# Kernel optimization log

Hardware: AMD Instinct MI355X
Metric: run time of the kernel (lower is better)

## Reference

```python
import jax, jax.numpy as jnp
import numpy as np

NUM_CLASSES = 7
CLASS_WEIGHT = 1.0
BOX_WEIGHT = 1.0


def _linear_sum_assignment(cost):
    """Exact Hungarian via shortest augmenting paths (Jonker-Volgenant style).
    Matches scipy.optimize.linear_sum_assignment for rectangular matrices:
    returns (row_ind, col_ind) of length min(n, m), row_ind sorted ascending."""
    C = np.asarray(cost, dtype=np.float64)
    transposed = C.shape[0] > C.shape[1]
    if transposed:
        C = C.T
    n, m = C.shape  # n <= m
    u = np.zeros(n + 1)
    v = np.zeros(m + 1)
    p = np.zeros(m + 1, dtype=np.int64)    # p[j]: row matched to col j (1-based); 0 = free
    way = np.zeros(m + 1, dtype=np.int64)
    for i in range(1, n + 1):
        p[0] = i
        j0 = 0
        minv = np.full(m + 1, np.inf)
        used = np.zeros(m + 1, dtype=bool)
        while True:
            used[j0] = True
            i0 = p[j0]
            cur = C[i0 - 1] - u[i0] - v[1:]
            free = ~used[1:]
            better = free & (cur < minv[1:])
            minv[1:][better] = cur[better]
            way[1:][better] = j0
            masked = np.where(free, minv[1:], np.inf)
            j0n = int(np.argmin(masked)) + 1
            delta = masked[j0n - 1]
            uj = np.nonzero(used)[0]
            u[p[uj]] += delta
            v[uj] -= delta
            minv[1:][free] -= delta
            j0 = j0n
            if p[j0] == 0:
                break
        while j0 != 0:   # augment along alternating path
            j1 = way[j0]
            p[j0] = p[j1]
            j0 = j1
    cols = np.nonzero(p[1:] > 0)[0]
    rows = p[1:][cols] - 1
    if transposed:
        rows, cols = cols, rows
    order = np.argsort(rows)
    return rows[order], cols[order]


def _cost_matrices(pred_logits, pred_boxes, gt_labels, gt_boxes):
    """Batched cost: class_weight * (-log_softmax gathered at gt labels) + box_weight * L1 cdist on xyz."""
    B, Q, _ = pred_logits.shape
    M = gt_labels.shape[1]
    log_probs = jax.nn.log_softmax(pred_logits, axis=-1)                       # (B,Q,C)
    idx = jnp.broadcast_to(gt_labels[:, None, :], (B, Q, M))
    class_cost = -jnp.take_along_axis(log_probs, idx, axis=2)                  # (B,Q,M)
    box_cost = jnp.sum(jnp.abs(pred_boxes[:, :, None, :3] - gt_boxes[:, None, :, :3]), axis=-1)  # (B,Q,M)
    return CLASS_WEIGHT * class_cost + BOX_WEIGHT * box_cost


def _matched_loss(pred_logits, pred_boxes, gt_labels, gt_boxes, rows, cols):
    B = pred_logits.shape[0]
    bidx = jnp.arange(B)[:, None]
    ml = pred_logits[bidx, rows]          # (B,M,C) matched logits
    mb = pred_boxes[bidx, rows]           # (B,M,7) matched boxes
    gl = gt_labels[bidx, cols]            # (B,M)
    gb = gt_boxes[bidx, cols]             # (B,M,7)
    logp = jax.nn.log_softmax(ml, axis=-1)
    ce = -jnp.mean(jnp.take_along_axis(logp, gl[..., None], axis=-1)[..., 0], axis=1)  # (B,)
    l1 = jnp.mean(jnp.abs(mb - gb), axis=(1, 2))                                       # (B,)
    return jnp.mean(CLASS_WEIGHT * ce + BOX_WEIGHT * l1)


def setup_inputs() -> dict:
    key = jax.random.key(0)
    k1, k2, k3, k4 = jax.random.split(key, 4)
    B, Q, M = 128, 900, 100
    return {
        'pred_logits': jax.random.normal(k1, (B, Q, NUM_CLASSES), dtype=jnp.float32),
        'pred_boxes': jax.random.normal(k2, (B, Q, 7), dtype=jnp.float32),
        'gt_labels': jax.random.randint(k3, (B, M), 0, NUM_CLASSES, dtype=jnp.int32),
        'gt_boxes': jax.random.normal(k4, (B, M, 7), dtype=jnp.float32),
    }


def reference(pred_logits, pred_boxes, gt_labels, gt_boxes):
    B = pred_logits.shape[0]
    M = gt_labels.shape[1]
    # Assignment is done on detached costs (host-side), matching the original module.
    cost = np.asarray(_cost_matrices(pred_logits, pred_boxes, gt_labels, gt_boxes))
    rows = np.zeros((B, M), dtype=np.int64)
    cols = np.zeros((B, M), dtype=np.int64)
    for b in range(B):
        r, c = _linear_sum_assignment(cost[b])
        rows[b], cols[b] = r, c
    return _matched_loss(pred_logits, pred_boxes, gt_labels, gt_boxes,
                         jnp.asarray(rows), jnp.asarray(cols))
```

## Files before the change

kernel.cpp:

```cpp
#include <hip/hip_runtime.h>
#include <math.h>


#define NQ   900
#define NG   100
#define NC   7
#define CPL  15
#define ROUNDS 10
#define INFF __builtin_inff()

__device__ __forceinline__ float readlane_f(float x, int l) {
  return __int_as_float(__builtin_amdgcn_readlane(__float_as_int(x), l));
}

template<int CTRL>
__device__ __forceinline__ void dpp_amin_step(float &v, int &ix) {
  float v2 = __int_as_float(__builtin_amdgcn_update_dpp(
      __float_as_int(v), __float_as_int(v), CTRL, 0xf, 0xf, false));
  int i2 = __builtin_amdgcn_update_dpp(ix, ix, CTRL, 0xf, 0xf, false);
  ix = (v2 < v) ? i2 : ix;
  v  = fminf(v, v2);
}
__device__ __forceinline__ void wave_amin_b(float v, int ix, float &ov, int &oi) {
  dpp_amin_step<0x111>(v, ix);
  dpp_amin_step<0x112>(v, ix);
  dpp_amin_step<0x114>(v, ix);
  dpp_amin_step<0x118>(v, ix);
  dpp_amin_step<0x142>(v, ix);
  dpp_amin_step<0x143>(v, ix);
  ov = readlane_f(v, 63);
  oi = __builtin_amdgcn_readlane(ix, 63);
}

template<int CTRL>
__device__ __forceinline__ void dpp_amin2_step(float &a, int &ia, float &b, int &ib) {
  const int INFI = 0x7f800000;
  float a2 = __int_as_float(__builtin_amdgcn_update_dpp(
      INFI, __float_as_int(a), CTRL, 0xf, 0xf, false));
  float b2 = __int_as_float(__builtin_amdgcn_update_dpp(
      INFI, __float_as_int(b), CTRL, 0xf, 0xf, false));
  int ia2 = __builtin_amdgcn_update_dpp(0, ia, CTRL, 0xf, 0xf, false);
  int ib2 = __builtin_amdgcn_update_dpp(0, ib, CTRL, 0xf, 0xf, false);
  bool sw = a2 < a;
  float hi = sw ? a  : a2;  int ihi = sw ? ia  : ia2;
  float lo = sw ? a2 : a;   int ilo = sw ? ia2 : ia;
  bool t1 = b2 < b;
  float bb = t1 ? b2 : b;   int ibb = t1 ? ib2 : ib;
  bool t2 = hi < bb;
  b = t2 ? hi : bb;         ib = t2 ? ihi : ibb;
  a = lo; ia = ilo;
}
__device__ __forceinline__ void wave_amin2_b(float a, int ia, float b, int ib,
    float &o1, int &oc1, float &o2, int &oc2) {
  dpp_amin2_step<0x111>(a, ia, b, ib);
  dpp_amin2_step<0x112>(a, ia, b, ib);
  dpp_amin2_step<0x114>(a, ia, b, ib);
  dpp_amin2_step<0x118>(a, ia, b, ib);
  dpp_amin2_step<0x142>(a, ia, b, ib);
  dpp_amin2_step<0x143>(a, ia, b, ib);
  o1 = readlane_f(a, 63); oc1 = __builtin_amdgcn_readlane(ia, 63);
  o2 = readlane_f(b, 63); oc2 = __builtin_amdgcn_readlane(ib, 63);
}

template<int CTRL>
__device__ __forceinline__ float dpp_add_step(float x) {
  int y = __builtin_amdgcn_update_dpp(0, __float_as_int(x),
                                      CTRL, 0xf, 0xf, true);
  return x + __int_as_float(y);
}
__device__ __forceinline__ float wave_sum_b(float x) {
  x = dpp_add_step<0x111>(x);
  x = dpp_add_step<0x112>(x);
  x = dpp_add_step<0x114>(x);
  x = dpp_add_step<0x118>(x);
  x = dpp_add_step<0x142>(x);
  x = dpp_add_step<0x143>(x);
  return __int_as_float(__builtin_amdgcn_readlane(__float_as_int(x), 63));
}
__device__ __forceinline__ void gl_lds16(const float* g, float* lds_base) {
  __builtin_amdgcn_global_load_lds(
      (const __attribute__((address_space(1))) unsigned int*)g,
      (__attribute__((address_space(3))) unsigned int*)lds_base, 16, 0, 0);
}
__device__ __forceinline__ float sel7v(float a0,float a1,float a2,float a3,
                                       float a4,float a5,float a6,int lab){
  float r = a0;
  r = lab==1 ? a1 : r;  r = lab==2 ? a2 : r;  r = lab==3 ? a3 : r;
  r = lab==4 ? a4 : r;  r = lab==5 ? a5 : r;  r = lab==6 ? a6 : r;
  return r;
}

__global__ __launch_bounds__(256, 1) void hungarian_fused_kernel(
    const float* __restrict__ logits, const float* __restrict__ pboxes,
    const int* __restrict__ glabels, const float* __restrict__ gboxes,
    float* __restrict__ out, float inv_B)
{
  const int b = blockIdx.x, tid = threadIdx.x;
  const int lane = tid & 63, w = tid >> 6;

  __shared__ __align__(16) float s_raw[NQ * NC];
  __shared__ __align__(16) float s_nlpT[NC * 1024];
  __shared__ __align__(16) float s_pb[960 * NC];
  __shared__ __align__(16) float s_gb[NG * NC];
  __shared__ __align__(16) int   s_glab[NG];
  __shared__ float s_u[NG + 1];
  __shared__ float s_v[CPL * 64];
  __shared__ int   s_p[NQ];
  __shared__ unsigned s_bid[NQ];
  __shared__ int   s_rmatch[NG];
  __shared__ float s_bm1[NG], s_bm2[NG];
  __shared__ int   s_bc[NG];
  __shared__ unsigned long long s_fm[2];
  __shared__ float s_f1v[NG]; __shared__ int s_f1c[NG];
  __shared__ float s_f2v[NG]; __shared__ int s_f2c[NG];
  __shared__ int   s_mlist[128];

  {
    const float* Lg = logits + (size_t)b * NQ * NC;
    const float* Pg = pboxes + (size_t)b * NQ * NC;
    const float* Gg = gboxes + (size_t)b * NG * NC;
    const int*   Bg = glabels + (size_t)b * NG;
    #pragma unroll
    for (int t = 0; t < 7; t++) {
      int i = (t << 8) + tid;
      if (i < (NQ * NC) / 4) {
        gl_lds16(Lg + i * 4, s_raw + ((t << 8) + (w << 6)) * 4);
        gl_lds16(Pg + i * 4, s_pb  + ((t << 8) + (w << 6)) * 4);
      }
    }
    if (tid < (NG * NC) / 4) gl_lds16(Gg + tid * 4, s_gb + (w << 6) * 4);
    if (tid < NG / 4) gl_lds16((const float*)Bg + tid * 4, (float*)s_glab);
    for (int i = tid; i < (960 - NQ) * NC; i += 256) s_pb[NQ * NC + i] = 0.f;
    for (int c = tid; c < NQ; c += 256) { s_p[c] = 0x7fffffff; s_bid[c] = 0xFFFFFFFFu; }
    for (int i = tid; i < CPL * 64; i += 256) s_v[i] = 0.f;
    if (tid == 0) s_u[0] = 0.f;
  }
  __syncthreads();

  for (int i = tid; i < 960; i += 256) {
    int L = i & 63, t = i >> 6;
    int q = L * CPL + t;
    float o[NC];
    if (q < NQ) {
      float x[NC];
      #pragma unroll
      for (int c = 0; c < NC; c++) x[c] = s_raw[q * NC + c];
      float mx = x[0];
      #pragma unroll
      for (int c = 1; c < NC; c++) mx = fmaxf(mx, x[c]);
      float tt[NC]; float se = 0.f;
      #pragma unroll
      for (int c = 0; c < NC; c++) { tt[c] = x[c] - mx; se += __expf(tt[c]); }
      float lg = __logf(se);
      #pragma unroll
      for (int c = 0; c < NC; c++) o[c] = lg - tt[c];
    } else {
      #pragma unroll
      for (int c = 0; c < NC; c++) o[c] = INFF;
    }
    #pragma unroll
    for (int c = 0; c < NC; c++) s_nlpT[c * 1024 + t * 64 + L] = o[c];
  }
  __syncthreads();

  const bool lval = (lane < NQ / CPL);
  float cpx[CPL], cpy[CPL], cpz[CPL];
  #pragma unroll
  for (int t = 0; t < CPL; t++) {
    int c = lane * CPL + t;
    cpx[t]=s_pb[c*NC+0]; cpy[t]=s_pb[c*NC+1]; cpz[t]=s_pb[c*NC+2];
  }

  for (int rl = 0; rl < 25; rl++) {
    int r = w * 25 + rl;
    int lab = s_glab[r];
    float gx = s_gb[r*NC+0], gy = s_gb[r*NC+1], gz = s_gb[r*NC+2];
    float m1 = INFF; int c1t = 0;
    #pragma unroll
    for (int t = 0; t < CPL; t++) {
      float nl = s_nlpT[lab*1024 + t*64 + lane];
      float bs = fabsf(cpx[t]-gx)+fabsf(cpy[t]-gy)+fabsf(cpz[t]-gz);
      float cost = nl + bs;
      bool lt1 = cost < m1;
      c1t = lt1 ? t : c1t;
      m1 = fminf(m1, cost);
    }
    float w1; int col;
    wave_amin_b(m1, lane * CPL + c1t, w1, col);
    if (lane == 0) {
      s_u[r + 1] = w1;
      s_bc[r] = col;
      atomicMin(&s_p[col], r + 1);
    }
  }
  __syncthreads();
  for (int c = tid; c < NQ; c += 256) if (s_p[c] == 0x7fffffff) s_p[c] = 0;
  if (tid < NG) {
    int c = s_bc[tid];
    s_rmatch[tid] = (s_p[c] == tid + 1) ? c + 1 : 0;
  }
  __syncthreads();

  for (int round = 0; round < ROUNDS; round++) {
    if (w == 0) {
      unsigned long long m = __ballot(s_rmatch[lane] == 0);
      if (lane == 0) s_fm[0] = m;
    } else if (w == 1) {
      unsigned long long m = __ballot((lane < NG - 64) && s_rmatch[64 + lane] == 0);
      if (lane == 0) s_fm[1] = m;
    }
    __syncthreads();
    const unsigned long long fm0r = s_fm[0], fm1r = s_fm[1];
    if ((fm0r | fm1r) == 0) break;
    float vreg[CPL];
    #pragma unroll
    for (int t = 0; t < CPL; t++) vreg[t] = s_v[t*64 + lane];
    {
      unsigned long long mm0 = fm0r, mm1 = fm1r;
      int idx = 0;
      while (mm0 | mm1) {
        int r;
        if (mm0) { int b2 = (int)__builtin_ctzll(mm0); mm0 &= mm0 - 1; r = b2; }
        else     { int b2 = (int)__builtin_ctzll(mm1); mm1 &= mm1 - 1; r = 64 + b2; }
        if ((idx++ & 3) != w) continue;
        int lab = s_glab[r];
        float gx = s_gb[r*NC+0], gy = s_gb[r*NC+1], gz = s_gb[r*NC+2];
        float m1 = INFF, m2 = INFF; int c1t = 0;
        #pragma unroll
        for (int t = 0; t < CPL; t++) {
          float nl = s_nlpT[lab*1024 + t*64 + lane];
          float bs = fabsf(cpx[t]-gx)+fabsf(cpy[t]-gy)+fabsf(cpz[t]-gz);
          float cost = (nl + bs) - vreg[t];
          bool lt1 = cost < m1;
          m2 = lt1 ? m1 : fminf(m2, cost);
// ... 78 lines not shown
                                : ((ff1 >> (tid - 64)) & 1ull);
      if (wasfree) {
        int c = s_bc[tid];
        if (s_p[c] == 0) atomicMin(&s_bid[c], (unsigned)tid);
      }
    }
    __syncthreads();
    if (tid < NG) {
      bool wasfree = (tid < 64) ? ((ff0 >> tid) & 1ull)
                                : ((ff1 >> (tid - 64)) & 1ull);
      if (wasfree) {
        int c = s_bc[tid];
        if (s_p[c] == 0 && s_bid[c] == (unsigned)tid) {
          s_p[c] = tid + 1;
          s_rmatch[tid] = c + 1;
        }
      }
    }
    __syncthreads();
    if (w == 0) {
      unsigned long long m = __ballot(s_rmatch[lane] == 0);
      if (lane == 0) s_fm[0] = m;
    } else if (w == 1) {
      unsigned long long m = __ballot((lane < NG - 64) && s_rmatch[64 + lane] == 0);
      if (lane == 0) s_fm[1] = m;
    }
    __syncthreads();
  }

  const unsigned long long gg0 = s_fm[0], gg1 = s_fm[1];
  const int nf2 = __popcll(gg0) + __popcll(gg1);

  if (nf2 > 0) {
  unsigned fmask = 0;
  if (lval) {
    #pragma unroll
    for (int t = 0; t < CPL; t++)
      if (s_p[lane * CPL + t] == 0) fmask |= (1u << t);
  }

  auto top2row = [&](int lab, float gx, float gy, float gz,
                     float &o1v, int &o1c, float &o2v, int &o2c) {
    float m1 = INFF, m2 = INFF; int c1 = 0, c2 = 0;
    #pragma unroll
    for (int t = 0; t < CPL; t++) {
      float nl = s_nlpT[lab*1024 + t*64 + lane];
      float bs = fabsf(cpx[t]-gx)+fabsf(cpy[t]-gy)+fabsf(cpz[t]-gz);
      float cost = nl + bs;
      cost = ((fmask >> t) & 1u) ? cost : INFF;
      bool lt1 = cost < m1;
      bool lt2 = cost < m2;
      c2 = lt1 ? c1 : (lt2 ? t : c2);
      m2 = lt1 ? m1 : fminf(m2, cost);
      c1 = lt1 ? t : c1;
      m1 = fminf(m1, cost);
    }
    wave_amin2_b(m1, lane * CPL + c1, m2, lane * CPL + c2, o1v, o1c, o2v, o2c);
  };

  for (int rl = 0; rl < 25; rl++) {
    int r = w * 25 + rl;
    int lab = s_glab[r];
    float gx = s_gb[r*NC+0], gy = s_gb[r*NC+1], gz = s_gb[r*NC+2];
    float v1, v2; int cc1, cc2;
    top2row(lab, gx, gy, gz, v1, cc1, v2, cc2);
    if (lane == 0) {
      s_f1v[r] = v1; s_f1c[r] = cc1; s_f2v[r] = v2; s_f2c[r] = cc2;
    }
  }
  __syncthreads();
  if (w != 0) return;

  volatile float* vu = s_u;

  const bool r1ok = (lane < NG - 64);
  int   rlab0 = s_glab[lane];
  float rgx0 = s_gb[lane*NC+0], rgy0 = s_gb[lane*NC+1], rgz0 = s_gb[lane*NC+2];
  int   rlab1 = 0; float rgx1=0.f, rgy1=0.f, rgz1=0.f;
  if (r1ok) {
    int r = 64 + lane;
    rlab1 = s_glab[r];
    rgx1 = s_gb[r*NC+0]; rgy1 = s_gb[r*NC+1]; rgz1 = s_gb[r*NC+2];
  }
  float ru0 = vu[lane + 1];
  float ru1 = r1ok ? vu[lane + 65] : 0.f;
  float rf1v0 = s_f1v[lane];       int rf1c0 = s_f1c[lane];
  float rf2v0 = s_f2v[lane];       int rf2c0 = s_f2c[lane];
  float rf1v1 = r1ok ? s_f1v[64+lane] : INFF; int rf1c1 = r1ok ? s_f1c[64+lane] : -1;
  float rf2v1 = r1ok ? s_f2v[64+lane] : INFF; int rf2c1 = r1ok ? s_f2c[64+lane] : -1;

  unsigned long long fm0 = gg0;
  unsigned long long fm1 = gg1;

  int NM = 0;
  #pragma unroll
  for (int t = 0; t < CPL; t++) {
    int c = lane * CPL + t;
    bool has = lval && (s_p[c] > 0);
    unsigned long long m = __ballot(has);
    int pos = NM + (int)__popcll(m & ((1ull << lane) - 1ull));
    if (has) s_mlist[pos] = c;
    NM += (int)__popcll(m);
  }

// ... 142 lines not shown
      ru0 = vu[lane + 1];
      if (r1ok) ru1 = vu[lane + 65];
      #pragma unroll
      for (int k = 0; k < 2; k++)
        if ((lane + (k << 6)) < NM) mpu[k] = vu[mprow[k]];

      if (lane == (jf / CPL)) fmask &= ~(1u << (jf - (jf / CPL) * CPL));
      if (rf1c0 == jf) { rf1v0 = rf2v0; rf1c0 = rf2c0; rf2c0 = -1; rf2v0 = INFF; }
      else if (rf2c0 == jf) { rf2c0 = -1; rf2v0 = INFF; }
      if (rf1c1 == jf) { rf1v1 = rf2v1; rf1c1 = rf2c1; rf2c1 = -1; rf2v1 = INFF; }
      else if (rf2c1 == jf) { rf2c1 = -1; rf2v1 = INFF; }
      unsigned long long need0 = __ballot(rf1c0 < 0);
      unsigned long long need1 = __ballot(r1ok && (rf1c1 < 0));
      while (need0) {
        int rb = (int)__builtin_ctzll(need0); need0 &= need0 - 1;
        int lab = __builtin_amdgcn_readlane(rlab0, rb);
        float gx = readlane_f(rgx0, rb), gy = readlane_f(rgy0, rb), gz = readlane_f(rgz0, rb);
        float v1, v2; int cc1, cc2;
        top2row(lab, gx, gy, gz, v1, cc1, v2, cc2);
        if (lane == rb) { rf1v0=v1; rf1c0=cc1; rf2v0=v2; rf2c0=cc2; }
      }
      while (need1) {
        int rb = (int)__builtin_ctzll(need1); need1 &= need1 - 1;
        int lab = __builtin_amdgcn_readlane(rlab1, rb);
        float gx = readlane_f(rgx1, rb), gy = readlane_f(rgy1, rb), gz = readlane_f(rgz1, rb);
        float v1, v2; int cc1, cc2;
        top2row(lab, gx, gy, gz, v1, cc1, v2, cc2);
        if (lane == rb) { rf1v1=v1; rf1c1=cc1; rf2v1=v2; rf2c1=cc2; }
      }
    }
  }
  }

  if (w != 0) return;
  {
    float ce = 0.f, l1 = 0.f;
    if (lval) {
      #pragma unroll
      for (int t = 0; t < CPL; t++) {
        int c = lane * CPL + t;
        int pr = s_p[c];
        if (pr > 0) {
          int g = pr - 1;
          int lg = s_glab[g];
          ce += s_nlpT[lg*1024 + t*64 + lane];
          float s = 0.f;
          #pragma unroll
          for (int d7 = 0; d7 < 7; d7++) s += fabsf(s_pb[c*NC+d7] - s_gb[g*NC+d7]);
          l1 += s;
        }
      }
    }
    float tot = ce * (1.f / NG) + l1 * (1.f / (NG * 7.f));
    tot = wave_sum_b(tot);
    if (lane == 0) atomicAdd(out, tot * inv_B);
  }
}

extern "C" void kernel_launch(void* const* d_in, const int* in_sizes, int n_in,
                              void* d_out, int out_size, void* d_ws, size_t ws_size,
                              hipStream_t stream) {
  const float* logits  = (const float*)d_in[0];
  const float* pboxes  = (const float*)d_in[1];
  const int*   glabels = (const int*)d_in[2];
  const float* gboxes  = (const float*)d_in[3];
  float* out = (float*)d_out;
  const int B = in_sizes[0] / (NQ * NC);

  hungarian_fused_kernel<<<dim3(B), dim3(256), 0, stream>>>(
      logits, pboxes, glabels, gboxes, out, 1.0f / (float)B);
}
```

Before: 129.3 us.

## Split fused Hungarian kernel into prep, auction and single-wave endgame kernels

Splits the single fused kernel into three launches that pass state through a global workspace. The first does log-softmax and the greedy initial assignment, the second runs the auction rounds and the top-2 precompute, and the third runs the serial endgame with a 64-thread block. The aim is to stop holding three idle waves per block during the serial single-wave endgame, with the old fused kernel kept as a fallback when the workspace is too small. In exchange it adds two extra launches and round trips of the LDS state through global memory, and with B=128 blocks on a large GPU occupancy may not be the limit, so it could be slower.

```diff
diff --git a/kernel.cpp b/kernel.cpp
--- a/kernel.cpp
+++ b/kernel.cpp
@@ -9,10 +9,20 @@
 #define ROUNDS 10
 #define INFF __builtin_inff()
 
+#define WS_STRIDE 9728
+#define WS_NLP 0
+#define WS_U   7168
+#define WS_P   7272
+#define WS_RM  8172
+#define WS_V   8272
+#define WS_F1V 9232
+#define WS_F1C 9332
+#define WS_F2V 9432
+#define WS_F2C 9532
+
 __device__ __forceinline__ float readlane_f(float x, int l) {
   return __int_as_float(__builtin_amdgcn_readlane(__float_as_int(x), l));
 }
-
 template<int CTRL>
 __device__ __forceinline__ void dpp_amin_step(float &v, int &ix) {
   float v2 = __int_as_float(__builtin_amdgcn_update_dpp(
@@ -31,7 +41,6 @@
   ov = readlane_f(v, 63);
   oi = __builtin_amdgcn_readlane(ix, 63);
 }
-
 template<int CTRL>
 __device__ __forceinline__ void dpp_amin2_step(float &a, int &ia, float &b, int &ib) {
   const int INFI = 0x7f800000;
@@ -61,7 +70,6 @@
   o1 = readlane_f(a, 63); oc1 = __builtin_amdgcn_readlane(ia, 63);
   o2 = readlane_f(b, 63); oc2 = __builtin_amdgcn_readlane(ib, 63);
 }
-
 template<int CTRL>
 __device__ __forceinline__ float dpp_add_step(float x) {
   int y = __builtin_amdgcn_update_dpp(0, __float_as_int(x),
@@ -90,15 +98,123 @@
   return r;
 }
 
-__global__ __launch_bounds__(256, 1) void hungarian_fused_kernel(
+__global__ __launch_bounds__(256, 1) void k_prep(
     const float* __restrict__ logits, const float* __restrict__ pboxes,
     const int* __restrict__ glabels, const float* __restrict__ gboxes,
-    float* __restrict__ out, float inv_B)
+    float* __restrict__ ws)
 {
   const int b = blockIdx.x, tid = threadIdx.x;
   const int lane = tid & 63, w = tid >> 6;
 
   __shared__ __align__(16) float s_raw[NQ * NC];
+  __shared__ __align__(16) float s_nlpT[NC * 1024];
+  __shared__ __align__(16) float s_pb[960 * NC];
+  __shared__ __align__(16) float s_gb[NG * NC];
+  __shared__ __align__(16) int   s_glab[NG];
+  __shared__ float s_u[NG + 1];
+  __shared__ int   s_p[NQ];
+  __shared__ int   s_bc[NG];
+  __shared__ int   s_rmatch[NG];
+
+  {
+    const float* Lg = logits + (size_t)b * NQ * NC;
+    const float* Pg = pboxes + (size_t)b * NQ * NC;
+    const float* Gg = gboxes + (size_t)b * NG * NC;
+    const int*   Bg = glabels + (size_t)b * NG;
+    #pragma unroll
+    for (int t = 0; t < 7; t++) {
+      int i = (t << 8) + tid;
+      if (i < (NQ * NC) / 4) {
+        gl_lds16(Lg + i * 4, s_raw + ((t << 8) + (w << 6)) * 4);
+        gl_lds16(Pg + i * 4, s_pb  + ((t << 8) + (w << 6)) * 4);
+      }
+    }
+    if (tid < (NG * NC) / 4) gl_lds16(Gg + tid * 4, s_gb + (w << 6) * 4);
+    if (tid < NG / 4) gl_lds16((const float*)Bg + tid * 4, (float*)s_glab);
+    for (int i = tid; i < (960 - NQ) * NC; i += 256) s_pb[NQ * NC + i] = 0.f;
+    for (int c = tid; c < NQ; c += 256) s_p[c] = 0x7fffffff;
+    if (tid == 0) s_u[0] = 0.f;
+  }
+  __syncthreads();
+
+  for (int i = tid; i < 960; i += 256) {
+    int L = i & 63, t = i >> 6;
+    int q = L * CPL + t;
+    float o[NC];
+    if (q < NQ) {
+      float x[NC];
+      #pragma unroll
+      for (int c = 0; c < NC; c++) x[c] = s_raw[q * NC + c];
+      float mx = x[0];
+      #pragma unroll
+      for (int c = 1; c < NC; c++) mx = fmaxf(mx, x[c]);
+      float tt[NC]; float se = 0.f;
+      #pragma unroll
+      for (int c = 0; c < NC; c++) { tt[c] = x[c] - mx; se += __expf(tt[c]); }
+      float lg = __logf(se);
+      #pragma unroll
+      for (int c = 0; c < NC; c++) o[c] = lg - tt[c];
+    } else {
+      #pragma unroll
+      for (int c = 0; c < NC; c++) o[c] = INFF;
+    }
+    #pragma unroll
+    for (int c = 0; c < NC; c++) s_nlpT[c * 1024 + t * 64 + L] = o[c];
+  }
+  __syncthreads();
+
+  float cpx[CPL], cpy[CPL], cpz[CPL];
+  #pragma unroll
+  for (int t = 0; t < CPL; t++) {
+    int c = lane * CPL + t;
+    cpx[t]=s_pb[c*NC+0]; cpy[t]=s_pb[c*NC+1]; cpz[t]=s_pb[c*NC+2];
+  }
+
+  for (int rl = 0; rl < 25; rl++) {
+    int r = w * 25 + rl;
+    int lab = s_glab[r];
+    float gx = s_gb[r*NC+0], gy = s_gb[r*NC+1], gz = s_gb[r*NC+2];
+    float m1 = INFF; int c1t = 0;
+    #pragma unroll
+    for (int t = 0; t < CPL; t++) {
+      float nl = s_nlpT[lab*1024 + t*64 + lane];
+      float bs = fabsf(cpx[t]-gx)+fabsf(cpy[t]-gy)+fabsf(cpz[t]-gz);
+      float cost = nl + bs;
+      bool lt1 = cost < m1;
+      c1t = lt1 ? t : c1t;
+      m1 = fminf(m1, cost);
+    }
+    float w1; int col;
+    wave_amin_b(m1, lane * CPL + c1t, w1, col);
+    if (lane == 0) {
+      s_u[r + 1] = w1;
+      s_bc[r] = col;
+      atomicMin(&s_p[col], r + 1);
+    }
+  }
+  __syncthreads();
+  for (int c = tid; c < NQ; c += 256) if (s_p[c] == 0x7fffffff) s_p[c] = 0;
+  if (tid < NG) {
+    int c = s_bc[tid];
+    s_rmatch[tid] = (s_p[c] == tid + 1) ? c + 1 : 0;
+  }
+  __syncthreads();
+
+  float* wsb = ws + (size_t)b * WS_STRIDE;
+  int*   wsi = (int*)wsb;
+  for (int i = tid; i < NC * 1024; i += 256) wsb[WS_NLP + i] = s_nlpT[i];
+  for (int i = tid; i <= NG; i += 256) wsb[WS_U + i] = s_u[i];
+  for (int i = tid; i < NQ; i += 256) wsi[WS_P + i] = s_p[i];
+  for (int i = tid; i < NG; i += 256) wsi[WS_RM + i] = s_rmatch[i];
+}
+
+__global__ __launch_bounds__(256, 1) void k_auction(
+    const float* __restrict__ pboxes, const int* __restrict__ glabels,
+    const float* __restrict__ gboxes, float* __restrict__ ws)
+{
+  const int b = blockIdx.x, tid = threadIdx.x;
+  const int lane = tid & 63, w = tid >> 6;
+
   __shared__ __align__(16) float s_nlpT[NC * 1024];
   __shared__ __align__(16) float s_pb[960 * NC];
   __shared__ __align__(16) float s_gb[NG * NC];
@@ -113,53 +229,27 @@
   __shared__ unsigned long long s_fm[2];
   __shared__ float s_f1v[NG]; __shared__ int s_f1c[NG];
   __shared__ float s_f2v[NG]; __shared__ int s_f2c[NG];
-  __shared__ int   s_mlist[128];
-
+
+  float* wsb = ws + (size_t)b * WS_STRIDE;
+  int*   wsi = (int*)wsb;
   {
-    const float* Lg = logits + (size_t)b * NQ * NC;
     const float* Pg = pboxes + (size_t)b * NQ * NC;
     const float* Gg = gboxes + (size_t)b * NG * NC;
     const int*   Bg = glabels + (size_t)b * NG;
     #pragma unroll
     for (int t = 0; t < 7; t++) {
       int i = (t << 8) + tid;
-      if (i < (NQ * NC) / 4) {
-        gl_lds16(Lg + i * 4, s_raw + ((t << 8) + (w << 6)) * 4);
-        gl_lds16(Pg + i * 4, s_pb  + ((t << 8) + (w << 6)) * 4);
-      }
+      gl_lds16(wsb + WS_NLP + i * 4, s_nlpT + ((t << 8) + (w << 6)) * 4);
+      if (i < (NQ * NC) / 4)
+        gl_lds16(Pg + i * 4, s_pb + ((t << 8) + (w << 6)) * 4);
     }
     if (tid < (NG * NC) / 4) gl_lds16(Gg + tid * 4, s_gb + (w << 6) * 4);
     if (tid < NG / 4) gl_lds16((const float*)Bg + tid * 4, (float*)s_glab);
     for (int i = tid; i < (960 - NQ) * NC; i += 256) s_pb[NQ * NC + i] = 0.f;
-    for (int c = tid; c < NQ; c += 256) { s_p[c] = 0x7fffffff; s_bid[c] = 0xFFFFFFFFu; }
+    for (int i = tid; i <= NG; i += 256) s_u[i] = wsb[WS_U + i];
+    for (int i = tid; i < NQ; i += 256) { s_p[i] = wsi[WS_P + i]; s_bid[i] = 0xFFFFFFFFu; }
+    for (int i = tid; i < NG; i += 256) s_rmatch[i] = wsi[WS_RM + i];
     for (int i = tid; i < CPL * 64; i += 256) s_v[i] = 0.f;
-    if (tid == 0) s_u[0] = 0.f;
-  }
-  __syncthreads();
-
-  for (int i = tid; i < 960; i += 256) {
-    int L = i & 63, t = i >> 6;
-    int q = L * CPL + t;
-    float o[NC];
-    if (q < NQ) {
-      float x[NC];
-      #pragma unroll
-      for (int c = 0; c < NC; c++) x[c] = s_raw[q * NC + c];
-      float mx = x[0];
-      #pragma unroll
-      for (int c = 1; c < NC; c++) mx = fmaxf(mx, x[c]);
-      float tt[NC]; float se = 0.f;
-      #pragma unroll
-      for (int c = 0; c < NC; c++) { tt[c] = x[c] - mx; se += __expf(tt[c]); }
-      float lg = __logf(se);
-      #pragma unroll
-      for (int c = 0; c < NC; c++) o[c] = lg - tt[c];
-    } else {
-      #pragma unroll
-      for (int c = 0; c < NC; c++) o[c] = INFF;
-    }
-    #pragma unroll
-    for (int c = 0; c < NC; c++) s_nlpT[c * 1024 + t * 64 + L] = o[c];
   }
   __syncthreads();
 
@@ -170,36 +260,6 @@
     int c = lane * CPL + t;
     cpx[t]=s_pb[c*NC+0]; cpy[t]=s_pb[c*NC+1]; cpz[t]=s_pb[c*NC+2];
   }
-
-  for (int rl = 0; rl < 25; rl++) {
-    int r = w * 25 + rl;
-    int lab = s_glab[r];
-    float gx = s_gb[r*NC+0], gy = s_gb[r*NC+1], gz = s_gb[r*NC+2];
-    float m1 = INFF; int c1t = 0;
-    #pragma unroll
-    for (int t = 0; t < CPL; t++) {
-      float nl = s_nlpT[lab*1024 + t*64 + lane];
-      float bs = fabsf(cpx[t]-gx)+fabsf(cpy[t]-gy)+fabsf(cpz[t]-gz);
-      float cost = nl + bs;
-      bool lt1 = cost < m1;
-      c1t = lt1 ? t : c1t;
-      m1 = fminf(m1, cost);
-    }
-    float w1; int col;
-    wave_amin_b(m1, lane * CPL + c1t, w1, col);
-    if (lane == 0) {
-      s_u[r + 1] = w1;
-      s_bc[r] = col;
-      atomicMin(&s_p[col], r + 1);
-    }
-  }
-  __syncthreads();
-  for (int c = tid; c < NQ; c += 256) if (s_p[c] == 0x7fffffff) s_p[c] = 0;
-  if (tid < NG) {
-    int c = s_bc[tid];
-    s_rmatch[tid] = (s_p[c] == tid + 1) ? c + 1 : 0;
-  }
-  __syncthreads();
 
   for (int round = 0; round < ROUNDS; round++) {
     if (w == 0) {
@@ -344,6 +404,115 @@
   const int nf2 = __popcll(gg0) + __popcll(gg1);
 
   if (nf2 > 0) {
+    unsigned fmask = 0;
+    if (lval) {
+      #pragma unroll
+      for (int t = 0; t < CPL; t++)
+        if (s_p[lane * CPL + t] == 0) fmask |= (1u << t);
+    }
+    for (int rl = 0; rl < 25; rl++) {
+      int r = w * 25 + rl;
+      int lab = s_glab[r];
+      float gx = s_gb[r*NC+0], gy = s_gb[r*NC+1], gz = s_gb[r*NC+2];
+      float m1 = INFF, m2 = INFF; int c1 = 0, c2 = 0;
+      #pragma unroll
+      for (int t = 0; t < CPL; t++) {
+        float nl = s_nlpT[lab*1024 + t*64 + lane];
+        float bs = fabsf(cpx[t]-gx)+fabsf(cpy[t]-gy)+fabsf(cpz[t]-gz);
+        float cost = nl + bs;
+        cost = ((fmask >> t) & 1u) ? cost : INFF;
+        bool lt1 = cost < m1;
+        bool lt2 = cost < m2;
+        c2 = lt1 ? c1 : (lt2 ? t : c2);
+        m2 = lt1 ? m1 : fminf(m2, cost);
+        c1 = lt1 ? t : c1;
+        m1 = fminf(m1, cost);
+      }
+      float v1, v2; int cc1, cc2;
+      wave_amin2_b(m1, lane * CPL + c1, m2, lane * CPL + c2, v1, cc1, v2, cc2);
+      if (lane == 0) {
+        s_f1v[r] = v1; s_f1c[r] = cc1; s_f2v[r] = v2; s_f2c[r] = cc2;
+      }
+    }
+    __syncthreads();
+  }
+
+  for (int i = tid; i <= NG; i += 256) wsb[WS_U + i] = s_u[i];
+  for (int i = tid; i < CPL * 64; i += 256) wsb[WS_V + i] = s_v[i];
+  for (int i = tid; i < NQ; i += 256) wsi[WS_P + i] = s_p[i];
+  for (int i = tid; i < NG; i += 256) wsi[WS_RM + i] = s_rmatch[i];
+  if (nf2 > 0) {
+    for (int i = tid; i < NG; i += 256) {
+      wsb[WS_F1V + i] = s_f1v[i]; wsi[WS_F1C + i] = s_f1c[i];
+      wsb[WS_F2V + i] = s_f2v[i]; wsi[WS_F2C + i] = s_f2c[i];
+    }
+  }
+}
+
+__global__ __launch_bounds__(64, 1) void k_endgame(
+    const float* __restrict__ pboxes, const int* __restrict__ glabels,
+    const float* __restrict__ gboxes, float* __restrict__ out, float inv_B,
+    float* __restrict__ ws)
+{
+  const int b = blockIdx.x, lane = threadIdx.x;
+
+  __shared__ __align__(16) float s_nlpT[NC * 1024];
+  __shared__ __align__(16) float s_pb[960 * NC];
+  __shared__ __align__(16) float s_gb[NG * NC];
+  __shared__ __align__(16) int   s_glab[NG];
+  __shared__ float s_u[NG + 1];
+  __shared__ float s_v[CPL * 64];
+  __shared__ int   s_p[NQ];
+  __shared__ int   s_rmatch[NG];
+  __shared__ float s_f1v[NG]; __shared__ int s_f1c[NG];
+  __shared__ float s_f2v[NG]; __shared__ int s_f2c[NG];
+  __shared__ int   s_mlist[128];
+
+  float* wsb = ws + (size_t)b * WS_STRIDE;
+  int*   wsi = (int*)wsb;
+  {
+    const float* Pg = pboxes + (size_t)b * NQ * NC;
+    const float* Gg = gboxes + (size_t)b * NG * NC;
+    const int*   Bg = glabels + (size_t)b * NG;
+    #pragma unroll
+    for (int it = 0; it < 28; it++)
+      gl_lds16(wsb + WS_NLP + (it * 64 + lane) * 4, s_nlpT + it * 256);
+    #pragma unroll
+    for (int it = 0; it < 25; it++) {
+      int i = it * 64 + lane;
+      if (i < (NQ * NC) / 4) gl_lds16(Pg + i * 4, s_pb + it * 256);
+    }
+    #pragma unroll
+    for (int it = 0; it < 3; it++) {
+      int i = it * 64 + lane;
+      if (i < (NG * NC) / 4) gl_lds16(Gg + i * 4, s_gb + it * 256);
+    }
+    if (lane < NG / 4) gl_lds16((const float*)Bg + lane * 4, (float*)s_glab);
+    for (int i = NQ * NC + lane; i < 960 * NC; i += 64) s_pb[i] = 0.f;
+    for (int i = lane; i <= NG; i += 64) s_u[i] = wsb[WS_U + i];
+    for (int i = lane; i < CPL * 64; i += 64) s_v[i] = wsb[WS_V + i];
+    for (int i = lane; i < NQ; i += 64) s_p[i] = wsi[WS_P + i];
+    for (int i = lane; i < NG; i += 64) {
+      s_rmatch[i] = wsi[WS_RM + i];
+      s_f1v[i] = wsb[WS_F1V + i]; s_f1c[i] = wsi[WS_F1C + i];
+      s_f2v[i] = wsb[WS_F2V + i]; s_f2c[i] = wsi[WS_F2C + i];
+    }
+  }
+  __syncthreads();
+
+  const unsigned long long gg0 = __ballot(s_rmatch[lane] == 0);
+  const unsigned long long gg1 = __ballot((lane < NG - 64) && s_rmatch[64 + lane] == 0);
+  const int nf2 = __popcll(gg0) + __popcll(gg1);
+
+  const bool lval = (lane < NQ / CPL);
+  float cpx[CPL], cpy[CPL], cpz[CPL];
+  #pragma unroll
+  for (int t = 0; t < CPL; t++) {
+    int c = lane * CPL + t;
+    cpx[t]=s_pb[c*NC+0]; cpy[t]=s_pb[c*NC+1]; cpz[t]=s_pb[c*NC+2];
+  }
+
+  if (nf2 > 0) {
   unsigned fmask = 0;
   if (lval) {
     #pragma unroll
@@ -369,19 +538,6 @@
     }
     wave_amin2_b(m1, lane * CPL + c1, m2, lane * CPL + c2, o1v, o1c, o2v, o2c);
   };
-
-  for (int rl = 0; rl < 25; rl++) {
-    int r = w * 25 + rl;
-    int lab = s_glab[r];
-    float gx = s_gb[r*NC+0], gy = s_gb[r*NC+1], gz = s_gb[r*NC+2];
-    float v1, v2; int cc1, cc2;
-    top2row(lab, gx, gy, gz, v1, cc1, v2, cc2);
-    if (lane == 0) {
-      s_f1v[r] = v1; s_f1c[r] = cc1; s_f2v[r] = v2; s_f2c[r] = cc2;
-    }
-  }
-  __syncthreads();
-  if (w != 0) return;
 
   volatile float* vu = s_u;
 
@@ -590,7 +746,6 @@
   }
   }
 
-  if (w != 0) return;
   {
     float ce = 0.f, l1 = 0.f;
     if (lval) {
@@ -615,6 +770,530 @@
   }
 }
 
+__global__ __launch_bounds__(256, 1) void hungarian_fused_kernel(
+    const float* __restrict__ logits, const float* __restrict__ pboxes,
+    const int* __restrict__ glabels, const float* __restrict__ gboxes,
+    float* __restrict__ out, float inv_B)
+{
+  const int b = blockIdx.x, tid = threadIdx.x;
+  const int lane = tid & 63, w = tid >> 6;
+
+  __shared__ __align__(16) float s_raw[NQ * NC];
+  __shared__ __align__(16) float s_nlpT[NC * 1024];
+  __shared__ __align__(16) float s_pb[960 * NC];
+  __shared__ __align__(16) float s_gb[NG * NC];
+  __shared__ __align__(16) int   s_glab[NG];
+  __shared__ float s_u[NG + 1];
+  __shared__ float s_v[CPL * 64];
+  __shared__ int   s_p[NQ];
+  __shared__ unsigned s_bid[NQ];
+  __shared__ int   s_rmatch[NG];
+  __shared__ float s_bm1[NG], s_bm2[NG];
+  __shared__ int   s_bc[NG];
+  __shared__ unsigned long long s_fm[2];
+  __shared__ float s_f1v[NG]; __shared__ int s_f1c[NG];
+  __shared__ float s_f2v[NG]; __shared__ int s_f2c[NG];
+  __shared__ int   s_mlist[128];
+
+  {
+    const float* Lg = logits + (size_t)b * NQ * NC;
+    const float* Pg = pboxes + (size_t)b * NQ * NC;
+    const float* Gg = gboxes + (size_t)b * NG * NC;
+    const int*   Bg = glabels + (size_t)b * NG;
+    #pragma unroll
+    for (int t = 0; t < 7; t++) {
+      int i = (t << 8) + tid;
+      if (i < (NQ * NC) / 4) {
+        gl_lds16(Lg + i * 4, s_raw + ((t << 8) + (w << 6)) * 4);
+        gl_lds16(Pg + i * 4, s_pb  + ((t << 8) + (w << 6)) * 4);
+      }
+    }
+    if (tid < (NG * NC) / 4) gl_lds16(Gg + tid * 4, s_gb + (w << 6) * 4);
+    if (tid < NG / 4) gl_lds16((const float*)Bg + tid * 4, (float*)s_glab);
+    for (int i = tid; i < (960 - NQ) * NC; i += 256) s_pb[NQ * NC + i] = 0.f;
+    for (int c = tid; c < NQ; c += 256) { s_p[c] = 0x7fffffff; s_bid[c] = 0xFFFFFFFFu; }
+    for (int i = tid; i < CPL * 64; i += 256) s_v[i] = 0.f;
+    if (tid == 0) s_u[0] = 0.f;
+  }
+  __syncthreads();
+
+  for (int i = tid; i < 960; i += 256) {
+    int L = i & 63, t = i >> 6;
+    int q = L * CPL + t;
+    float o[NC];
+    if (q < NQ) {
+      float x[NC];
+      #pragma unroll
+      for (int c = 0; c < NC; c++) x[c] = s_raw[q * NC + c];
+      float mx = x[0];
+      #pragma unroll
+      for (int c = 1; c < NC; c++) mx = fmaxf(mx, x[c]);
+      float tt[NC]; float se = 0.f;
+      #pragma unroll
+      for (int c = 0; c < NC; c++) { tt[c] = x[c] - mx; se += __expf(tt[c]); }
+      float lg = __logf(se);
+      #pragma unroll
+      for (int c = 0; c < NC; c++) o[c] = lg - tt[c];
+    } else {
+      #pragma unroll
+      for (int c = 0; c < NC; c++) o[c] = INFF;
+    }
+    #pragma unroll
+    for (int c = 0; c < NC; c++) s_nlpT[c * 1024 + t * 64 + L] = o[c];
+  }
+  __syncthreads();
+
+  const bool lval = (lane < NQ / CPL);
+  float cpx[CPL], cpy[CPL], cpz[CPL];
+  #pragma unroll
+  for (int t = 0; t < CPL; t++) {
+    int c = lane * CPL + t;
+    cpx[t]=s_pb[c*NC+0]; cpy[t]=s_pb[c*NC+1]; cpz[t]=s_pb[c*NC+2];
+  }
+
+  for (int rl = 0; rl < 25; rl++) {
+    int r = w * 25 + rl;
+    int lab = s_glab[r];
+    float gx = s_gb[r*NC+0], gy = s_gb[r*NC+1], gz = s_gb[r*NC+2];
+    float m1 = INFF; int c1t = 0;
+    #pragma unroll
+    for (int t = 0; t < CPL; t++) {
+      float nl = s_nlpT[lab*1024 + t*64 + lane];
+      float bs = fabsf(cpx[t]-gx)+fabsf(cpy[t]-gy)+fabsf(cpz[t]-gz);
+      float cost = nl + bs;
+      bool lt1 = cost < m1;
+      c1t = lt1 ? t : c1t;
+      m1 = fminf(m1, cost);
+    }
+    float w1; int col;
+    wave_amin_b(m1, lane * CPL + c1t, w1, col);
+    if (lane == 0) {
+      s_u[r + 1] = w1;
+      s_bc[r] = col;
+      atomicMin(&s_p[col], r + 1);
+    }
+  }
+  __syncthreads();
+  for (int c = tid; c < NQ; c += 256) if (s_p[c] == 0x7fffffff) s_p[c] = 0;
+  if (tid < NG) {
+    int c = s_bc[tid];
+    s_rmatch[tid] = (s_p[c] == tid + 1) ? c + 1 : 0;
+  }
+  __syncthreads();
+
+  for (int round = 0; round < ROUNDS; round++) {
+    if (w == 0) {
+      unsigned long long m = __ballot(s_rmatch[lane] == 0);
+      if (lane == 0) s_fm[0] = m;
+    } else if (w == 1) {
+      unsigned long long m = __ballot((lane < NG - 64) && s_rmatch[64 + lane] == 0);
+      if (lane == 0) s_fm[1] = m;
+    }
+    __syncthreads();
+    const unsigned long long fm0r = s_fm[0], fm1r = s_fm[1];
+    if ((fm0r | fm1r) == 0) break;
+    float vreg[CPL];
+    #pragma unroll
+    for (int t = 0; t < CPL; t++) vreg[t] = s_v[t*64 + lane];
+    {
+      unsigned long long mm0 = fm0r, mm1 = fm1r;
+      int idx = 0;
+      while (mm0 | mm1) {
+        int r;
+        if (mm0) { int b2 = (int)__builtin_ctzll(mm0); mm0 &= mm0 - 1; r = b2; }
+        else     { int b2 = (int)__builtin_ctzll(mm1); mm1 &= mm1 - 1; r = 64 + b2; }
+        if ((idx++ & 3) != w) continue;
+        int lab = s_glab[r];
+        float gx = s_gb[r*NC+0], gy = s_gb[r*NC+1], gz = s_gb[r*NC+2];
+        float m1 = INFF, m2 = INFF; int c1t = 0;
+        #pragma unroll
+        for (int t = 0; t < CPL; t++) {
+          float nl = s_nlpT[lab*1024 + t*64 + lane];
+          float bs = fabsf(cpx[t]-gx)+fabsf(cpy[t]-gy)+fabsf(cpz[t]-gz);
+          float cost = (nl + bs) - vreg[t];
+          bool lt1 = cost < m1;
+          m2 = lt1 ? m1 : fminf(m2, cost);
+          c1t = lt1 ? t : c1t;
+          m1 = fminf(m1, cost);
+        }
+        float w1, w2; int col1, dumc;
+        wave_amin2_b(m1, lane * CPL + c1t, m2, 0, w1, col1, w2, dumc);
+        if (lane == 0) {
+          s_bm1[r] = w1; s_bm2[r] = w2; s_bc[r] = col1;
+          atomicMin(&s_bid[col1],
+                    (__float_as_uint(w1) & 0xFFFFFF80u) | (unsigned)(r + 1));
+        }
+      }
+    }
+    __syncthreads();
+    if (tid < NG) {
+      bool wasfree = (tid < 64) ? ((fm0r >> tid) & 1ull)
+                                : ((fm1r >> (tid - 64)) & 1ull);
+      if (wasfree) {
+        int c = s_bc[tid];
+        if ((s_bid[c] & 0x7Fu) == (unsigned)(tid + 1)) {
+          int dold = s_p[c];
+          s_p[c] = tid + 1;
+          s_rmatch[tid] = c + 1;
+          if (dold > 0) s_rmatch[dold - 1] = 0;
+          s_u[tid + 1] = s_bm2[tid];
+          s_v[(c % CPL) * 64 + (c / CPL)] -= (s_bm2[tid] - s_bm1[tid]);
+        }
+      }
+    }
+    __syncthreads();
+    if (tid < NG) {
+      bool wasfree = (tid < 64) ? ((fm0r >> tid) & 1ull)
+                                : ((fm1r >> (tid - 64)) & 1ull);
+      if (wasfree) s_bid[s_bc[tid]] = 0xFFFFFFFFu;
+    }
+  }
+  __syncthreads();
+
+  if (w == 0) {
+    unsigned long long m = __ballot(s_rmatch[lane] == 0);
+    if (lane == 0) s_fm[0] = m;
+  } else if (w == 1) {
+    unsigned long long m = __ballot((lane < NG - 64) && s_rmatch[64 + lane] == 0);
+    if (lane == 0) s_fm[1] = m;
+  }
+  __syncthreads();
+  const unsigned long long ff0 = s_fm[0], ff1 = s_fm[1];
+  const int nfinal = __popcll(ff0) + __popcll(ff1);
+  if (nfinal > 0) {
+    float vreg[CPL];
+    #pragma unroll
+    for (int t = 0; t < CPL; t++) vreg[t] = s_v[t*64 + lane];
+    unsigned long long mm0 = ff0, mm1 = ff1;
+    int idx = 0;
+    while (mm0 | mm1) {
+      int r;
+      if (mm0) { int b2 = (int)__builtin_ctzll(mm0); mm0 &= mm0 - 1; r = b2; }
+      else     { int b2 = (int)__builtin_ctzll(mm1); mm1 &= mm1 - 1; r = 64 + b2; }
+      if ((idx++ & 3) != w) continue;
+      int lab = s_glab[r];
+      float gx = s_gb[r*NC+0], gy = s_gb[r*NC+1], gz = s_gb[r*NC+2];
+      float m1 = INFF; int c1t = 0;
+      #pragma unroll
+      for (int t = 0; t < CPL; t++) {
+        float nl = s_nlpT[lab*1024 + t*64 + lane];
+        float bs = fabsf(cpx[t]-gx)+fabsf(cpy[t]-gy)+fabsf(cpz[t]-gz);
+        float cost = (nl + bs) - vreg[t];
+        bool lt1 = cost < m1;
+        c1t = lt1 ? t : c1t;
+        m1 = fminf(m1, cost);
+      }
+      float w1; int col;
+      wave_amin_b(m1, lane * CPL + c1t, w1, col);
+      if (lane == 0) { s_u[r + 1] = w1; s_bc[r] = col; }
+    }
+    __syncthreads();
+    if (tid < NG) {
+      bool wasfree = (tid < 64) ? ((ff0 >> tid) & 1ull)
+                                : ((ff1 >> (tid - 64)) & 1ull);
+      if (wasfree) {
+        int c = s_bc[tid];
+        if (s_p[c] == 0) atomicMin(&s_bid[c], (unsigned)tid);
+      }
+    }
+    __syncthreads();
+    if (tid < NG) {
+      bool wasfree = (tid < 64) ? ((ff0 >> tid) & 1ull)
+                                : ((ff1 >> (tid - 64)) & 1ull);
+      if (wasfree) {
+        int c = s_bc[tid];
+        if (s_p[c] == 0 && s_bid[c] == (unsigned)tid) {
+          s_p[c] = tid + 1;
+          s_rmatch[tid] = c + 1;
+        }
+      }
+    }
+    __syncthreads();
+    if (w == 0) {
+      unsigned long long m = __ballot(s_rmatch[lane] == 0);
+      if (lane == 0) s_fm[0] = m;
+    } else if (w == 1) {
+      unsigned long long m = __ballot((lane < NG - 64) && s_rmatch[64 + lane] == 0);
+      if (lane == 0) s_fm[1] = m;
+    }
+    __syncthreads();
+  }
+
+  const unsigned long long gg0 = s_fm[0], gg1 = s_fm[1];
+  const int nf2 = __popcll(gg0) + __popcll(gg1);
+
+  if (nf2 > 0) {
+  unsigned fmask = 0;
+  if (lval) {
+    #pragma unroll
+    for (int t = 0; t < CPL; t++)
+      if (s_p[lane * CPL + t] == 0) fmask |= (1u << t);
+  }
+
+  auto top2row = [&](int lab, float gx, float gy, float gz,
+                     float &o1v, int &o1c, float &o2v, int &o2c) {
+    float m1 = INFF, m2 = INFF; int c1 = 0, c2 = 0;
+    #pragma unroll
+    for (int t = 0; t < CPL; t++) {
+      float nl = s_nlpT[lab*1024 + t*64 + lane];
+      float bs = fabsf(cpx[t]-gx)+fabsf(cpy[t]-gy)+fabsf(cpz[t]-gz);
+      float cost = nl + bs;
+      cost = ((fmask >> t) & 1u) ? cost : INFF;
+      bool lt1 = cost < m1;
+      bool lt2 = cost < m2;
+      c2 = lt1 ? c1 : (lt2 ? t : c2);
+      m2 = lt1 ? m1 : fminf(m2, cost);
+      c1 = lt1 ? t : c1;
+      m1 = fminf(m1, cost);
+    }
+    wave_amin2_b(m1, lane * CPL + c1, m2, lane * CPL + c2, o1v, o1c, o2v, o2c);
+  };
+
+  for (int rl = 0; rl < 25; rl++) {
+    int r = w * 25 + rl;
+    int lab = s_glab[r];
+    float gx = s_gb[r*NC+0], gy = s_gb[r*NC+1], gz = s_gb[r*NC+2];
+    float v1, v2; int cc1, cc2;
+    top2row(lab, gx, gy, gz, v1, cc1, v2, cc2);
+    if (lane == 0) {
+      s_f1v[r] = v1; s_f1c[r] = cc1; s_f2v[r] = v2; s_f2c[r] = cc2;
+    }
+  }
+  __syncthreads();
+  if (w != 0) return;
+
+  volatile float* vu = s_u;
+
+  const bool r1ok = (lane < NG - 64);
+  int   rlab0 = s_glab[lane];
+  float rgx0 = s_gb[lane*NC+0], rgy0 = s_gb[lane*NC+1], rgz0 = s_gb[lane*NC+2];
+  int   rlab1 = 0; float rgx1=0.f, rgy1=0.f, rgz1=0.f;
+  if (r1ok) {
+    int r = 64 + lane;
+    rlab1 = s_glab[r];
+    rgx1 = s_gb[r*NC+0]; rgy1 = s_gb[r*NC+1]; rgz1 = s_gb[r*NC+2];
+  }
+  float ru0 = vu[lane + 1];
+  float ru1 = r1ok ? vu[lane + 65] : 0.f;
+  float rf1v0 = s_f1v[lane];       int rf1c0 = s_f1c[lane];
+  float rf2v0 = s_f2v[lane];       int rf2c0 = s_f2c[lane];
+  float rf1v1 = r1ok ? s_f1v[64+lane] : INFF; int rf1c1 = r1ok ? s_f1c[64+lane] : -1;
+  float rf2v1 = r1ok ? s_f2v[64+lane] : INFF; int rf2c1 = r1ok ? s_f2c[64+lane] : -1;
+
+  unsigned long long fm0 = gg0;
+  unsigned long long fm1 = gg1;
+
+  int NM = 0;
+  #pragma unroll
+  for (int t = 0; t < CPL; t++) {
+    int c = lane * CPL + t;
+    bool has = lval && (s_p[c] > 0);
+    unsigned long long m = __ballot(has);
+    int pos = NM + (int)__popcll(m & ((1ull << lane) - 1ull));
+    if (has) s_mlist[pos] = c;
+    NM += (int)__popcll(m);
+  }
+
+  int   mcol[2]  = {-1,-1};
+  int   mprow[2] = {0,0};
+  float mpu[2]   = {0.f,0.f};
+  float mv[2]    = {0.f,0.f};
+  float mx[2]={0,0}, my[2]={0,0}, mz[2]={0,0};
+  float mn0[2],mn1[2],mn2[2],mn3[2],mn4[2],mn5[2],mn6[2];
+  #pragma unroll
+  for (int k = 0; k < 2; k++) { mn0[k]=0;mn1[k]=0;mn2[k]=0;mn3[k]=0;mn4[k]=0;mn5[k]=0;mn6[k]=0; }
+  #pragma unroll
+  for (int k = 0; k < 2; k++) {
+    int s = lane + (k << 6);
+    if (s < NM) {
+      int c = s_mlist[s];
+      int cq = c / CPL, ct = c - cq * CPL;
+      mcol[k] = c;
+      mx[k] = s_pb[c*NC+0]; my[k] = s_pb[c*NC+1]; mz[k] = s_pb[c*NC+2];
+      mn0[k] = s_nlpT[0*1024 + ct*64 + cq];
+      mn1[k] = s_nlpT[1*1024 + ct*64 + cq];
+      mn2[k] = s_nlpT[2*1024 + ct*64 + cq];
+      mn3[k] = s_nlpT[3*1024 + ct*64 + cq];
+      mn4[k] = s_nlpT[4*1024 + ct*64 + cq];
+      mn5[k] = s_nlpT[5*1024 + ct*64 + cq];
+      mn6[k] = s_nlpT[6*1024 + ct*64 + cq];
+      mprow[k] = s_p[c];
+      mpu[k] = vu[mprow[k]];
+      mv[k] = s_v[ct * 64 + cq];
+    }
+  }
+
+  float dsl[2]; int wsl[2];
+
+  for (int half = 0; half < 2; half++) {
+    unsigned long long fm = half ? fm1 : fm0;
+    while (fm) {
+      int bit = (int)__builtin_ctzll(fm);
+      fm &= fm - 1;
+      int rfree = bit + (half ? 65 : 1);
+      dsl[0] = INFF; dsl[1] = INFF; wsl[0] = 0; wsl[1] = 0;
+      unsigned usedm = 0;
+      float bfv = INFF; int bfc = -1, bfprev = 0;
+      int i0 = rfree;
+      int ro0 = rfree - 1;
+      float u_i0 = readlane_f((ro0 >> 6) ? ru1 : ru0, ro0 & 63);
+      int j0p = 0;
+      float minVal = 0.f;
+      int jf = -1, jfprev = 0;
+
+      for (int it = 0; it < 128; it++) {
+        int ro = i0 - 1, rown = ro & 63, rs = ro >> 6;
+        int   lab = __builtin_amdgcn_readlane(rs ? rlab1 : rlab0, rown);
+        float gx = readlane_f(rs ? rgx1 : rgx0, rown);
+        float gy = readlane_f(rs ? rgy1 : rgy0, rown);
+        float gz = readlane_f(rs ? rgz1 : rgz0, rown);
+        float hs = minVal - u_i0;
+        float f1v = readlane_f(rs ? rf1v1 : rf1v0, rown);
+        int   f1c = __builtin_amdgcn_readlane(rs ? rf1c1 : rf1c0, rown);
+        float cbf = f1v + hs;
+        if (cbf < bfv) { bfv = cbf; bfc = f1c; bfprev = j0p; }
+        float lb = INFF; int bk = 0;
+        #pragma unroll
+        for (int k = 0; k < 2; k++) {
+          bool gate = ((lane + (k << 6)) < NM) && !((usedm >> k) & 1u);
+          float nl = sel7v(mn0[k],mn1[k],mn2[k],mn3[k],mn4[k],mn5[k],mn6[k],lab);
+          float bs = fabsf(mx[k]-gx)+fabsf(my[k]-gy)+fabsf(mz[k]-gz);
+          float rr = ((nl + bs) + hs) - mv[k];
+          bool imp = gate && (rr < dsl[k]);
+          dsl[k] = imp ? rr : dsl[k];
+          wsl[k] = imp ? j0p : wsl[k];
+          float cand = gate ? dsl[k] : INFF;
+          bool bt = cand < lb;
+          bk = bt ? k : bk;
+          lb = fminf(lb, cand);
+        }
+        float dm; int spk;
+        wave_amin_b(lb, (bk << 6) | lane, dm, spk);
+        if (bfv <= dm) { minVal = bfv; jf = bfc; jfprev = bfprev; break; }
+        minVal = dm;
+        int so = spk & 63, sk = spk >> 6;
+        usedm |= (lane == so) ? (1u << sk) : 0u;
+        i0  = __builtin_amdgcn_readlane(sk ? mprow[1] : mprow[0], so);
+        u_i0 = readlane_f(sk ? mpu[1] : mpu[0], so);
+        j0p = spk + 1;
+      }
+      if (jf < 0) { jf = bfc; jfprev = bfprev; minVal = bfv; }
+
+      if (lane == 0) vu[rfree] += minVal;
+      #pragma unroll
+      for (int k = 0; k < 2; k++) {
+        if ((usedm >> k) & 1u) {
+          float a = minVal - dsl[k];
+          mv[k] -= a;
+          vu[mprow[k]] += a;
+        }
+      }
+      __threadfence_block();
+
+      int pred = jfprev;
+      int nr;
+      if (pred == 0) nr = rfree;
+      else {
+        int s = pred - 1;
+        nr = __builtin_amdgcn_readlane((s >> 6) ? mprow[1] : mprow[0], s & 63);
+      }
+      if (lane == 0) s_p[jf] = nr;
+      {
+        int cq = jf / CPL, ct = jf - cq * CPL;
+        float nx = s_pb[jf*NC+0], ny = s_pb[jf*NC+1], nz = s_pb[jf*NC+2];
+        float a0 = s_nlpT[0*1024 + ct*64 + cq];
+        float a1 = s_nlpT[1*1024 + ct*64 + cq];
+        float a2 = s_nlpT[2*1024 + ct*64 + cq];
+        float a3 = s_nlpT[3*1024 + ct*64 + cq];
+        float a4 = s_nlpT[4*1024 + ct*64 + cq];
+        float a5 = s_nlpT[5*1024 + ct*64 + cq];
+        float a6 = s_nlpT[6*1024 + ct*64 + cq];
+        int kk = NM >> 6;
+        if (lane == (NM & 63) && NM < 128) {
+          if (kk == 0) {
+            mcol[0]=jf; mx[0]=nx; my[0]=ny; mz[0]=nz; mprow[0]=nr; mv[0]=0.f;
+            mn0[0]=a0;mn1[0]=a1;mn2[0]=a2;mn3[0]=a3;mn4[0]=a4;mn5[0]=a5;mn6[0]=a6;
+          } else {
+            mcol[1]=jf; mx[1]=nx; my[1]=ny; mz[1]=nz; mprow[1]=nr; mv[1]=0.f;
+            mn0[1]=a0;mn1[1]=a1;mn2[1]=a2;mn3[1]=a3;mn4[1]=a4;mn5[1]=a5;mn6[1]=a6;
+          }
+        }
+        NM++;
+      }
+      while (pred) {
+        int s = pred - 1, so = s & 63, sk = s >> 6;
+        int np = __builtin_amdgcn_readlane(sk ? wsl[1] : wsl[0], so);
+        int nr2;
+        if (np == 0) nr2 = rfree;
+        else {
+          int s2 = np - 1;
+          nr2 = __builtin_amdgcn_readlane((s2 >> 6) ? mprow[1] : mprow[0], s2 & 63);
+        }
+        int sc = __builtin_amdgcn_readlane(sk ? mcol[1] : mcol[0], so);
+        if (lane == so) { if (sk) mprow[1] = nr2; else mprow[0] = nr2; }
+        if (lane == 0) s_p[sc] = nr2;
+        pred = np;
+      }
+      __threadfence_block();
+
+      ru0 = vu[lane + 1];
+      if (r1ok) ru1 = vu[lane + 65];
+      #pragma unroll
+      for (int k = 0; k < 2; k++)
+        if ((lane + (k << 6)) < NM) mpu[k] = vu[mprow[k]];
+
+      if (lane == (jf / CPL)) fmask &= ~(1u << (jf - (jf / CPL) * CPL));
+      if (rf1c0 == jf) { rf1v0 = rf2v0; rf1c0 = rf2c0; rf2c0 = -1; rf2v0 = INFF; }
+      else if (rf2c0 == jf) { rf2c0 = -1; rf2v0 = INFF; }
+      if (rf1c1 == jf) { rf1v1 = rf2v1; rf1c1 = rf2c1; rf2c1 = -1; rf2v1 = INFF; }
+      else if (rf2c1 == jf) { rf2c1 = -1; rf2v1 = INFF; }
+      unsigned long long need0 = __ballot(rf1c0 < 0);
+      unsigned long long need1 = __ballot(r1ok && (rf1c1 < 0));
+      while (need0) {
+        int rb = (int)__builtin_ctzll(need0); need0 &= need0 - 1;
+        int lab = __builtin_amdgcn_readlane(rlab0, rb);
+        float gx = readlane_f(rgx0, rb), gy = readlane_f(rgy0, rb), gz = readlane_f(rgz0, rb);
+        float v1, v2; int cc1, cc2;
+        top2row(lab, gx, gy, gz, v1, cc1, v2, cc2);
+        if (lane == rb) { rf1v0=v1; rf1c0=cc1; rf2v0=v2; rf2c0=cc2; }
+      }
+      while (need1) {
+        int rb = (int)__builtin_ctzll(need1); need1 &= need1 - 1;
+        int lab = __builtin_amdgcn_readlane(rlab1, rb);
+        float gx = readlane_f(rgx1, rb), gy = readlane_f(rgy1, rb), gz = readlane_f(rgz1, rb);
+        float v1, v2; int cc1, cc2;
+        top2row(lab, gx, gy, gz, v1, cc1, v2, cc2);
+        if (lane == rb) { rf1v1=v1; rf1c1=cc1; rf2v1=v2; rf2c1=cc2; }
+      }
+    }
+  }
+  }
+
+  if (w != 0) return;
+  {
+    float ce = 0.f, l1 = 0.f;
+    if (lval) {
+      #pragma unroll
+      for (int t = 0; t < CPL; t++) {
+        int c = lane * CPL + t;
+        int pr = s_p[c];
+        if (pr > 0) {
+          int g = pr - 1;
+          int lg = s_glab[g];
+          ce += s_nlpT[lg*1024 + t*64 + lane];
+          float s = 0.f;
+          #pragma unroll
+          for (int d7 = 0; d7 < 7; d7++) s += fabsf(s_pb[c*NC+d7] - s_gb[g*NC+d7]);
+          l1 += s;
+        }
+      }
+    }
+    float tot = ce * (1.f / NG) + l1 * (1.f / (NG * 7.f));
+    tot = wave_sum_b(tot);
+    if (lane == 0) atomicAdd(out, tot * inv_B);
+  }
+}
+
 extern "C" void kernel_launch(void* const* d_in, const int* in_sizes, int n_in,
                               void* d_out, int out_size, void* d_ws, size_t ws_size,
                               hipStream_t stream) {
@@ -625,6 +1304,15 @@
   float* out = (float*)d_out;
   const int B = in_sizes[0] / (NQ * NC);
 
-  hungarian_fused_kernel<<<dim3(B), dim3(256), 0, stream>>>(
-      logits, pboxes, glabels, gboxes, out, 1.0f / (float)B);
+  const size_t need = (size_t)B * WS_STRIDE * sizeof(float);
+  if (d_ws != nullptr && ws_size >= need) {
+    float* ws = (float*)d_ws;
+    k_prep<<<dim3(B), dim3(256), 0, stream>>>(logits, pboxes, glabels, gboxes, ws);
+    k_auction<<<dim3(B), dim3(256), 0, stream>>>(pboxes, glabels, gboxes, ws);
+    k_endgame<<<dim3(B), dim3(64), 0, stream>>>(pboxes, glabels, gboxes, out,
+                                                1.0f / (float)B, ws);
+  } else {
+    hungarian_fused_kernel<<<dim3(B), dim3(256), 0, stream>>>(
+        logits, pboxes, glabels, gboxes, out, 1.0f / (float)B);
+  }
 }
```

Measured after the change: 147.1 us. 1.14x slower.
